# Optimization experiments

Measured on AMD Instinct MI355X. Metric: run time of the kernel, lower is better.

## Reference

```python
import jax, jax.numpy as jnp
import numpy as np

EMBED_DIM = 1024
NUM_HEADS = 16
HEAD_DIM = EMBED_DIM // NUM_HEADS
LN_EPS = 1e-5


def setup_inputs() -> dict:
    key = jax.random.key(0)
    ks = jax.random.split(key, 6)
    b, s, d = 2, 2048, EMBED_DIM
    scale = 1.0 / np.sqrt(d)
    x = jax.random.normal(ks[0], (b, s, d), dtype=jnp.float32)
    w_qkv = jax.random.normal(ks[1], (d, 3 * d), dtype=jnp.float32) * scale
    b_qkv = jax.random.normal(ks[2], (3 * d,), dtype=jnp.float32) * 0.02
    w_out = jax.random.normal(ks[3], (d, d), dtype=jnp.float32) * scale
    b_out = jax.random.normal(ks[4], (d,), dtype=jnp.float32) * 0.02
    gamma = jnp.ones((d,), dtype=jnp.float32)
    ln_beta = jnp.zeros((d,), dtype=jnp.float32)
    beta = jax.random.normal(ks[5], (), dtype=jnp.float32) * 0.1
    return {"x": x, "w_qkv": w_qkv, "b_qkv": b_qkv, "w_out": w_out,
            "b_out": b_out, "gamma": gamma, "ln_beta": ln_beta, "beta": beta}


def _layernorm(x, gamma, ln_beta):
    mu = jnp.mean(x, axis=-1, keepdims=True)
    var = jnp.mean(jnp.square(x - mu), axis=-1, keepdims=True)
    return (x - mu) * jax.lax.rsqrt(var + LN_EPS) * gamma + ln_beta


def reference(x, w_qkv, b_qkv, w_out, b_out, gamma, ln_beta, beta):
    b, s, d = x.shape
    h, hd = NUM_HEADS, HEAD_DIM
    residual = x
    xn = _layernorm(x, gamma, ln_beta)
    qkv = xn @ w_qkv + b_qkv                       # [b, s, 3d]
    qkv = qkv.reshape(b, s, 3, h, hd)
    q = jnp.transpose(qkv[:, :, 0], (0, 2, 1, 3))  # [b, h, s, hd]
    k = jnp.transpose(qkv[:, :, 1], (0, 2, 1, 3))
    v = jnp.transpose(qkv[:, :, 2], (0, 2, 1, 3))
    attn = jnp.einsum('bhqd,bhkd->bhqk', q, k) / np.sqrt(hd)
    idx = jnp.arange(s)
    dist = jnp.abs(idx[None, :] - idx[:, None]).astype(attn.dtype)  # [s, s]
    attn = attn + beta * jnp.log1p(dist)[None, None, :, :]
    probs = jax.nn.softmax(attn, axis=-1)
    ctx = jnp.einsum('bhqk,bhkd->bhqd', probs, v)  # [b, h, s, hd]
    ctx = jnp.transpose(ctx, (0, 2, 1, 3)).reshape(b, s, d)
    return residual + ctx @ w_out + b_out
```

## Files before the change

kernel.cpp:

```cpp
#include <hip/hip_runtime.h>

#define SEQ 2048
#define DIM 1024
#define NHEAD 16
#define HDIM 64
#define NTOK 4096
#define N3D 3072

typedef __attribute__((ext_vector_type(8))) short bf16x8;
typedef __attribute__((ext_vector_type(4))) float floatx4;
typedef __attribute__((ext_vector_type(4))) unsigned short ushortx4;

__device__ __forceinline__ unsigned short f2bf(float f) {
    unsigned int u = __builtin_bit_cast(unsigned int, f);
    u += 0x7FFFu + ((u >> 16) & 1u);
    return (unsigned short)(u >> 16);
}

__device__ __forceinline__ void async_copy16(const void* g, const void* l) {
    __builtin_amdgcn_global_load_lds(
        (const __attribute__((address_space(1))) unsigned int*)(unsigned long long)g,
        (__attribute__((address_space(3))) unsigned int*)(unsigned int)(unsigned long long)l,
        16, 0, 0);
}

#define MFMA_BF16(a, b, c) __builtin_amdgcn_mfma_f32_16x16x32_bf16((a), (b), (c), 0, 0, 0)

__global__ __launch_bounds__(256)
void prep_kernel(const float* __restrict__ w_qkv, unsigned short* __restrict__ wqkvT,
                 const float* __restrict__ w_out, unsigned short* __restrict__ woutT,
                 const float* __restrict__ x, const float* __restrict__ gamma,
                 const float* __restrict__ lnb, unsigned short* __restrict__ xn,
                 const float* __restrict__ betap, float* __restrict__ logt_g) {
    const int bid = blockIdx.x;
    const int tid = threadIdx.x;
    if (bid >= 8192) {
        const float betaV = betap[0];
        const float L2E = 1.44269504f;
        int i = (bid - 8192) * 256 + tid;
        logt_g[i] = betaV * log1pf((float)i) * L2E - 20.0f;
        logt_g[i + 1024] = betaV * log1pf((float)(i + 1024)) * L2E - 20.0f;
        return;
    }
    if (bid < 4096) {
        __shared__ float tile[32][33];
        const float* src; unsigned short* dst; int cols, bx, by;
        if (bid < 3072) { src = w_qkv; dst = wqkvT; cols = N3D; bx = bid % 96; by = bid / 96; }
        else { int t = bid - 3072; src = w_out; dst = woutT; cols = DIM; bx = t & 31; by = t >> 5; }
        const int c0 = bx * 32, r0 = by * 32;
        const int tx = tid & 31, ty = tid >> 5;
        for (int i = 0; i < 4; ++i) {
            int r = ty + i * 8;
            tile[r][tx] = src[(size_t)(r0 + r) * cols + c0 + tx];
        }
        __syncthreads();
        for (int i = 0; i < 4; ++i) {
            int rr = ty + i * 8;
            dst[(size_t)(c0 + rr) * DIM + r0 + tx] = f2bf(tile[tx][rr]);
        }
    } else {
        const int row = bid - 4096;
        const float* xr = x + (size_t)row * DIM;
        float4 v = ((const float4*)xr)[tid];
        float s = v.x + v.y + v.z + v.w;
        float s2 = v.x * v.x + v.y * v.y + v.z * v.z + v.w * v.w;
        for (int off = 1; off < 64; off <<= 1) {
            s += __shfl_xor(s, off, 64);
            s2 += __shfl_xor(s2, off, 64);
        }
        __shared__ float red[8];
        const int wave = tid >> 6, lane = tid & 63;
        if (lane == 0) { red[wave] = s; red[4 + wave] = s2; }
        __syncthreads();
        s = red[0] + red[1] + red[2] + red[3];
        s2 = red[4] + red[5] + red[6] + red[7];
        const float mu = s * (1.0f / DIM);
        const float var = s2 * (1.0f / DIM) - mu * mu;
        const float rstd = rsqrtf(var + 1e-5f);
        float4 g = ((const float4*)gamma)[tid];
        float4 bb = ((const float4*)lnb)[tid];
        unsigned short* o = xn + (size_t)row * DIM + tid * 4;
        o[0] = f2bf((v.x - mu) * rstd * g.x + bb.x);
        o[1] = f2bf((v.y - mu) * rstd * g.y + bb.y);
        o[2] = f2bf((v.z - mu) * rstd * g.z + bb.z);
        o[3] = f2bf((v.w - mu) * rstd * g.w + bb.w);
    }
}

__global__ __launch_bounds__(256)
void qkv_gemm(const unsigned short* __restrict__ A, const unsigned short* __restrict__ Bt,
              const float* __restrict__ bias, unsigned short* __restrict__ qo,
              unsigned short* __restrict__ ko, unsigned short* __restrict__ vTo) {
    __shared__ unsigned short Asm[2][128 * 64];
    __shared__ unsigned short Bsm[2][192 * 64];
    const int tid = threadIdx.x;
    const int wave = tid >> 6, lane = tid & 63;
    const int quad = lane >> 4, r16 = lane & 15;
    const int flat = blockIdx.x;
    const int xcd = flat & 7, c = flat >> 3;
    const int mt = (xcd >> 1) * 8 + (c >> 3);
    const int nt = (xcd & 1) * 8 + (c & 7);
    const int m0 = mt * 128, n0 = nt * 192;
    const int wm = (wave & 1) * 64, wn = (wave >> 1) * 96;
    floatx4 acc[4][6] = {};
    for (int p = 0; p < 4; ++p) {
        int s = tid + p * 256;
        async_copy16(A + (size_t)(m0 + (s >> 3)) * DIM + ((s & 7) << 3), &Asm[0][s * 8]);
    }
    for (int p = 0; p < 6; ++p) {
        int s = tid + p * 256;
        async_copy16(Bt + (size_t)(n0 + (s >> 3)) * DIM + ((s & 7) << 3), &Bsm[0][s * 8]);
    }
    __syncthreads();
    for (int it = 0; it < 16; ++it) {
        const int cur = it & 1;
        if (it + 1 < 16) {
            const int k1 = (it + 1) * 64;
            for (int p = 0; p < 4; ++p) {
                int s = tid + p * 256;
                async_copy16(A + (size_t)(m0 + (s >> 3)) * DIM + k1 + ((s & 7) << 3),
                             &Asm[cur ^ 1][s * 8]);
            }
            for (int p = 0; p < 6; ++p) {
                int s = tid + p * 256;
                async_copy16(Bt + (size_t)(n0 + (s >> 3)) * DIM + k1 + ((s & 7) << 3),
                             &Bsm[cur ^ 1][s * 8]);
            }
        }
        for (int h = 0; h < 2; ++h) {
            bf16x8 af[4], bfr[6];
            for (int i = 0; i < 4; ++i)
                af[i] = *(const bf16x8*)(&Asm[cur][(wm + i * 16 + r16) * 64 + h * 32 + quad * 8]);
            for (int j = 0; j < 6; ++j)
                bfr[j] = *(const bf16x8*)(&Bsm[cur][(wn + j * 16 + r16) * 64 + h * 32 + quad * 8]);
            for (int i = 0; i < 4; ++i)
                for (int j = 0; j < 6; ++j)
                    acc[i][j] = MFMA_BF16(af[i], bfr[j], acc[i][j]);
        }
        __syncthreads();
    }
    for (int j = 0; j < 6; ++j) {
        int n = n0 + wn + j * 16 + r16;
        float bn = bias[n];
        int part = n >> 10, nn = n & 1023;
        int head = nn >> 6, hdi = nn & 63;
        for (int i = 0; i < 4; ++i) {
            int mbase = m0 + wm + i * 16 + quad * 4;
            int bIdx = mbase >> 11, sIdx = mbase & 2047;
            if (part == 2) {
                ushortx4 pack;
                for (int e = 0; e < 4; ++e) pack[e] = f2bf(acc[i][j][e] + bn);
                *(ushortx4*)(vTo + ((size_t)(bIdx * NHEAD + head) * HDIM + hdi) * SEQ + sIdx) = pack;
            } else {
                unsigned short* dst = (part == 0) ? qo : ko;
                for (int e = 0; e < 4; ++e)
                    dst[((size_t)(bIdx * NHEAD + head) * SEQ + sIdx + e) * HDIM + hdi] =
                        f2bf(acc[i][j][e] + bn);
            }
        }
    }
}

__global__ __launch_bounds__(512)
void attn_kernel(const unsigned short* __restrict__ qg, const unsigned short* __restrict__ kg,
                 const unsigned short* __restrict__ vTg, const float* __restrict__ logt,
                 unsigned short* __restrict__ ctx) {
    __shared__ unsigned short QP[128][72];
    __shared__ unsigned short Kd[2][64 * 64];
    __shared__ unsigned short Vd[2][64 * 64];

    const int tid = threadIdx.x;
    const int wave = tid >> 6, lane = tid & 63;
    const int quad = lane >> 4, r16 = lane & 15;
    const int flat = blockIdx.y * 16 + blockIdx.x;
    const int swz = (flat & 7) * 64 + (flat >> 3);
    const int bh = swz >> 4, qt = swz & 15;
    const int qBase = qt * 128;
    const float L2E = 1.44269504f;
    const float c1 = 0.125f * L2E;

    const unsigned short* qptr = qg + ((size_t)bh * SEQ + qBase) * HDIM;
    for (int s = tid; s < 1024; s += 512) {
        int r = s >> 3, c8 = (s & 7) << 3;
        *(bf16x8*)(&QP[r][c8]) = *(const bf16x8*)(qptr + r * HDIM + c8);
    }

    const int sr = tid >> 3;
    const int scg = (tid & 7) ^ (sr & 7);
    const unsigned short* kbh = kg + (size_t)bh * SEQ * HDIM;
    const unsigned short* vbh = vTg + (size_t)bh * HDIM * SEQ;
    async_copy16(kbh + (size_t)sr * HDIM + scg * 8, &Kd[0][tid * 8]);
    async_copy16(vbh + (size_t)sr * SEQ + scg * 8, &Vd[0][tid * 8]);
    __syncthreads();

    bf16x8 qf0 = *(const bf16x8*)(&QP[wave * 16 + r16][quad * 8]);
    bf16x8 qf1 = *(const bf16x8*)(&QP[wave * 16 + r16][32 + quad * 8]);

    const bf16x8 onesv = {0x3F80, 0x3F80, 0x3F80, 0x3F80, 0x3F80, 0x3F80, 0x3F80, 0x3F80};

    floatx4 o[5] = {};
    const int qWaveBase = qBase + wave * 16;
    const int qrT = qWaveBase + r16;

    for (int kt0 = 0; kt0 < SEQ; kt0 += 64) {
        const int buf = (kt0 >> 6) & 1;
        if (kt0 + 64 < SEQ) {
            async_copy16(kbh + (size_t)(kt0 + 64 + sr) * HDIM + scg * 8, &Kd[buf ^ 1][tid * 8]);
            async_copy16(vbh + (size_t)sr * SEQ + kt0 + 64 + scg * 8, &Vd[buf ^ 1][tid * 8]);
        }

        floatx4 sc[4];
        __builtin_amdgcn_s_setprio(1);
        for (int ct = 0; ct < 4; ++ct) {
            int rK = ct * 16 + r16;
            const unsigned short* kb = &Kd[buf][rK * 64];
            bf16x8 kf0 = *(const bf16x8*)(kb + ((quad ^ (rK & 7)) << 3));
            bf16x8 kf1 = *(const bf16x8*)(kb + (((quad ^ 4) ^ (rK & 7)) << 3));
            floatx4 z = {0.f, 0.f, 0.f, 0.f};
            z = MFMA_BF16(kf0, qf0, z);
            z = MFMA_BF16(kf1, qf1, z);
            sc[ct] = z;
        }
        __builtin_amdgcn_s_setprio(0);
        for (int ct = 0; ct < 4; ++ct) {
            const int keyTile = kt0 + ct * 16;
            const int kbase = keyTile + quad * 4;
            if (qWaveBase >= keyTile + 16) {
                const float* lp = &logt[qrT - kbase - 3];
                for (int i = 0; i < 4; ++i)
                    sc[ct][i] = __builtin_amdgcn_exp2f(sc[ct][i] * c1 + lp[3 - i]);
            } else if (keyTile >= qWaveBase + 16) {
                const float* lp = &logt[kbase - qrT];
                for (int i = 0; i < 4; ++i)
                    sc[ct][i] = __builtin_amdgcn_exp2f(sc[ct][i] * c1 + lp[i]);
            } else {
                for (int i = 0; i < 4; ++i) {
                    int dist = qrT - (kbase + i);
                    dist = dist < 0 ? -dist : dist;
                    sc[ct][i] = __builtin_amdgcn_exp2f(sc[ct][i] * c1 + logt[dist]);
                }
            }
        }
        {
            unsigned short* prow = &QP[wave * 16 + r16][0];
            for (int ct = 0; ct < 4; ++ct) {
                unsigned int lo, hi;
                asm("v_cvt_pk_bf16_f32 %0, %1, %2" : "=v"(lo) : "v"(sc[ct][0]), "v"(sc[ct][1]));
                asm("v_cvt_pk_bf16_f32 %0, %1, %2" : "=v"(hi) : "v"(sc[ct][2]), "v"(sc[ct][3]));
                uint2 pk; pk.x = lo; pk.y = hi;
                *(uint2*)(prow + ct * 16 + quad * 4) = pk;
            }
        }
        bf16x8 pf0 = *(const bf16x8*)(&QP[wave * 16 + r16][quad * 8]);
        bf16x8 pf1 = *(const bf16x8*)(&QP[wave * 16 + r16][32 + quad * 8]);
        __builtin_amdgcn_s_setprio(1);
        for (int nt = 0; nt < 4; ++nt) {
            int rV = nt * 16 + r16;
            const unsigned short* vb = &Vd[buf][rV * 64];
            bf16x8 vf0 = *(const bf16x8*)(vb + ((quad ^ (rV & 7)) << 3));
            bf16x8 vf1 = *(const bf16x8*)(vb + (((quad ^ 4) ^ (rV & 7)) << 3));
            o[nt] = MFMA_BF16(pf0, vf0, o[nt]);
            o[nt] = MFMA_BF16(pf1, vf1, o[nt]);
        }
        o[4] = MFMA_BF16(pf0, onesv, o[4]);
        o[4] = MFMA_BF16(pf1, onesv, o[4]);
        __builtin_amdgcn_s_setprio(0);

        __syncthreads();
    }

    const int b_ = bh >> 4, h_ = bh & 15;
    for (int i = 0; i < 4; ++i) {
        float inv = 1.0f / o[4][i];
        int qi = qBase + wave * 16 + quad * 4 + i;
        for (int nt = 0; nt < 4; ++nt) {
            int d = nt * 16 + r16;
            ctx[((size_t)(b_ * SEQ + qi)) * DIM + h_ * HDIM + d] = f2bf(o[nt][i] * inv);
        }
    }
}

__global__ __launch_bounds__(256)
void out_gemm(const unsigned short* __restrict__ A, const unsigned short* __restrict__ Bt,
              const float* __restrict__ bias, const float* __restrict__ resid,
              float* __restrict__ out) {
    __shared__ unsigned short Asm[2][128 * 64];
    __shared__ unsigned short Bsm[2][64 * 64];
    const int tid = threadIdx.x;
    const int wave = tid >> 6, lane = tid & 63;
    const int quad = lane >> 4, r16 = lane & 15;
    const int flat = blockIdx.y * 16 + blockIdx.x;
    const int swz = (flat & 7) * 64 + (flat >> 3);
    const int m0 = (swz >> 4) * 128, n0 = (swz & 15) * 64;
    const int wm = (wave & 1) * 64, wn = (wave >> 1) * 32;
    floatx4 acc[4][2] = {};
    for (int p = 0; p < 4; ++p) {
        int s = tid + p * 256;
        async_copy16(A + (size_t)(m0 + (s >> 3)) * DIM + ((s & 7) << 3), &Asm[0][s * 8]);
    }
    for (int p = 0; p < 2; ++p) {
        int s = tid + p * 256;
        async_copy16(Bt + (size_t)(n0 + (s >> 3)) * DIM + ((s & 7) << 3), &Bsm[0][s * 8]);
    }
    __syncthreads();
    for (int it = 0; it < 16; ++it) {
        const int cur = it & 1;
        if (it + 1 < 16) {
            const int k1 = (it + 1) * 64;
            for (int p = 0; p < 4; ++p) {
                int s = tid + p * 256;
                async_copy16(A + (size_t)(m0 + (s >> 3)) * DIM + k1 + ((s & 7) << 3),
                             &Asm[cur ^ 1][s * 8]);
            }
            for (int p = 0; p < 2; ++p) {
                int s = tid + p * 256;
                async_copy16(Bt + (size_t)(n0 + (s >> 3)) * DIM + k1 + ((s & 7) << 3),
                             &Bsm[cur ^ 1][s * 8]);
            }
        }
        for (int h = 0; h < 2; ++h) {
            bf16x8 af[4], bfr[2];
            for (int i = 0; i < 4; ++i)
                af[i] = *(const bf16x8*)(&Asm[cur][(wm + i * 16 + r16) * 64 + h * 32 + quad * 8]);
            for (int j = 0; j < 2; ++j)
                bfr[j] = *(const bf16x8*)(&Bsm[cur][(wn + j * 16 + r16) * 64 + h * 32 + quad * 8]);
            for (int i = 0; i < 4; ++i)
                for (int j = 0; j < 2; ++j)
                    acc[i][j] = MFMA_BF16(af[i], bfr[j], acc[i][j]);
        }
        __syncthreads();
    }
    for (int i = 0; i < 4; ++i)
        for (int j = 0; j < 2; ++j)
            for (int e = 0; e < 4; ++e) {
                int m = m0 + wm + i * 16 + quad * 4 + e;
                int n = n0 + wn + j * 16 + r16;
                out[(size_t)m * DIM + n] = acc[i][j][e] + bias[n] + resid[(size_t)m * DIM + n];
            }
}

extern "C" void kernel_launch(void* const* d_in, const int* in_sizes, int n_in,
                              void* d_out, int out_size, void* d_ws, size_t ws_size,
                              hipStream_t stream) {
    const float* x     = (const float*)d_in[0];
    const float* w_qkv = (const float*)d_in[1];
    const float* b_qkv = (const float*)d_in[2];
    const float* w_out = (const float*)d_in[3];
    const float* b_out = (const float*)d_in[4];
    const float* gamma = (const float*)d_in[5];
    const float* ln_b  = (const float*)d_in[6];
    const float* beta  = (const float*)d_in[7];
    float* out = (float*)d_out;

    char* ws = (char*)d_ws;
    const size_t MB = 1u << 20;
    unsigned short* xn    = (unsigned short*)(ws);
    unsigned short* wqkvT = (unsigned short*)(ws + 8 * MB);
    unsigned short* woutT = (unsigned short*)(ws + 14 * MB);
    unsigned short* qb    = (unsigned short*)(ws + 16 * MB);
    unsigned short* kb    = (unsigned short*)(ws + 24 * MB);
    unsigned short* vTb   = (unsigned short*)(ws + 32 * MB);
    float* logt_g         = (float*)(ws + 40 * MB);
    unsigned short* ctx   = xn;

    prep_kernel<<<8196, 256, 0, stream>>>(w_qkv, wqkvT, w_out, woutT, x, gamma, ln_b, xn,
                                          beta, logt_g);
    qkv_gemm<<<512, 256, 0, stream>>>(xn, wqkvT, b_qkv, qb, kb, vTb);
    attn_kernel<<<dim3(SEQ / 128, 32), 512, 0, stream>>>(qb, kb, vTb, logt_g, ctx);
    out_gemm<<<dim3(16, 32), 256, 0, stream>>>(ctx, woutT, b_out, x, out);
}
```

Before: 219.0 us.

## Shrink attention blocks to 64 query rows and swizzle the P scratch buffer

After: 224.0 us. +2.3%, slower.

```diff
diff --git a/kernel.cpp b/kernel.cpp
--- a/kernel.cpp
+++ b/kernel.cpp
@@ -161,52 +161,56 @@
     }
 }
 
-__global__ __launch_bounds__(512)
+__global__ __launch_bounds__(256)
 void attn_kernel(const unsigned short* __restrict__ qg, const unsigned short* __restrict__ kg,
                  const unsigned short* __restrict__ vTg, const float* __restrict__ logt,
                  unsigned short* __restrict__ ctx) {
-    __shared__ unsigned short QP[128][72];
+    __shared__ unsigned short QP[64][64];
     __shared__ unsigned short Kd[2][64 * 64];
     __shared__ unsigned short Vd[2][64 * 64];
 
     const int tid = threadIdx.x;
     const int wave = tid >> 6, lane = tid & 63;
     const int quad = lane >> 4, r16 = lane & 15;
-    const int flat = blockIdx.y * 16 + blockIdx.x;
-    const int swz = (flat & 7) * 64 + (flat >> 3);
-    const int bh = swz >> 4, qt = swz & 15;
-    const int qBase = qt * 128;
+    const int flat = blockIdx.x;
+    const int swz = (flat & 7) * 128 + (flat >> 3);
+    const int bh = swz >> 5, qt = swz & 31;
+    const int qBase = qt * 64;
     const float L2E = 1.44269504f;
     const float c1 = 0.125f * L2E;
 
     const unsigned short* qptr = qg + ((size_t)bh * SEQ + qBase) * HDIM;
-    for (int s = tid; s < 1024; s += 512) {
-        int r = s >> 3, c8 = (s & 7) << 3;
-        *(bf16x8*)(&QP[r][c8]) = *(const bf16x8*)(qptr + r * HDIM + c8);
-    }
-
-    const int sr = tid >> 3;
-    const int scg = (tid & 7) ^ (sr & 7);
+    const int qrow = wave * 16 + r16;
+    bf16x8 qf0 = *(const bf16x8*)(qptr + qrow * HDIM + quad * 8);
+    bf16x8 qf1 = *(const bf16x8*)(qptr + qrow * HDIM + 32 + quad * 8);
+
     const unsigned short* kbh = kg + (size_t)bh * SEQ * HDIM;
     const unsigned short* vbh = vTg + (size_t)bh * HDIM * SEQ;
-    async_copy16(kbh + (size_t)sr * HDIM + scg * 8, &Kd[0][tid * 8]);
-    async_copy16(vbh + (size_t)sr * SEQ + scg * 8, &Vd[0][tid * 8]);
+    for (int p = 0; p < 2; ++p) {
+        int s = tid + p * 256;
+        int sr = s >> 3, scg = (s & 7) ^ (sr & 7);
+        async_copy16(kbh + (size_t)sr * HDIM + scg * 8, &Kd[0][s * 8]);
+        async_copy16(vbh + (size_t)sr * SEQ + scg * 8, &Vd[0][s * 8]);
+    }
     __syncthreads();
-
-    bf16x8 qf0 = *(const bf16x8*)(&QP[wave * 16 + r16][quad * 8]);
-    bf16x8 qf1 = *(const bf16x8*)(&QP[wave * 16 + r16][32 + quad * 8]);
 
     const bf16x8 onesv = {0x3F80, 0x3F80, 0x3F80, 0x3F80, 0x3F80, 0x3F80, 0x3F80, 0x3F80};
 
     floatx4 o[5] = {};
     const int qWaveBase = qBase + wave * 16;
     const int qrT = qWaveBase + r16;
+    const int rx = r16 & 7;
+    unsigned short* prow = &QP[wave * 16 + r16][0];
 
     for (int kt0 = 0; kt0 < SEQ; kt0 += 64) {
         const int buf = (kt0 >> 6) & 1;
         if (kt0 + 64 < SEQ) {
-            async_copy16(kbh + (size_t)(kt0 + 64 + sr) * HDIM + scg * 8, &Kd[buf ^ 1][tid * 8]);
-            async_copy16(vbh + (size_t)sr * SEQ + kt0 + 64 + scg * 8, &Vd[buf ^ 1][tid * 8]);
+            for (int p = 0; p < 2; ++p) {
+                int s = tid + p * 256;
+                int sr = s >> 3, scg = (s & 7) ^ (sr & 7);
+                async_copy16(kbh + (size_t)(kt0 + 64 + sr) * HDIM + scg * 8, &Kd[buf ^ 1][s * 8]);
+                async_copy16(vbh + (size_t)sr * SEQ + kt0 + 64 + scg * 8, &Vd[buf ^ 1][s * 8]);
+            }
         }
 
         floatx4 sc[4];
@@ -241,18 +245,16 @@
                 }
             }
         }
-        {
-            unsigned short* prow = &QP[wave * 16 + r16][0];
-            for (int ct = 0; ct < 4; ++ct) {
-                unsigned int lo, hi;
-                asm("v_cvt_pk_bf16_f32 %0, %1, %2" : "=v"(lo) : "v"(sc[ct][0]), "v"(sc[ct][1]));
-                asm("v_cvt_pk_bf16_f32 %0, %1, %2" : "=v"(hi) : "v"(sc[ct][2]), "v"(sc[ct][3]));
-                uint2 pk; pk.x = lo; pk.y = hi;
-                *(uint2*)(prow + ct * 16 + quad * 4) = pk;
-            }
-        }
-        bf16x8 pf0 = *(const bf16x8*)(&QP[wave * 16 + r16][quad * 8]);
-        bf16x8 pf1 = *(const bf16x8*)(&QP[wave * 16 + r16][32 + quad * 8]);
+        for (int ct = 0; ct < 4; ++ct) {
+            unsigned int lo, hi;
+            asm("v_cvt_pk_bf16_f32 %0, %1, %2" : "=v"(lo) : "v"(sc[ct][0]), "v"(sc[ct][1]));
+            asm("v_cvt_pk_bf16_f32 %0, %1, %2" : "=v"(hi) : "v"(sc[ct][2]), "v"(sc[ct][3]));
+            uint2 pk; pk.x = lo; pk.y = hi;
+            int slot = (2 * ct + (quad >> 1)) ^ rx;
+            *(uint2*)((char*)prow + slot * 16 + (quad & 1) * 8) = pk;
+        }
+        bf16x8 pf0 = *(const bf16x8*)((const char*)prow + ((quad ^ rx) * 16));
+        bf16x8 pf1 = *(const bf16x8*)((const char*)prow + (((4 + quad) ^ rx) * 16));
         __builtin_amdgcn_s_setprio(1);
         for (int nt = 0; nt < 4; ++nt) {
             int rV = nt * 16 + r16;
@@ -366,6 +368,6 @@
     prep_kernel<<<8196, 256, 0, stream>>>(w_qkv, wqkvT, w_out, woutT, x, gamma, ln_b, xn,
                                           beta, logt_g);
     qkv_gemm<<<512, 256, 0, stream>>>(xn, wqkvT, b_qkv, qb, kb, vTb);
-    attn_kernel<<<dim3(SEQ / 128, 32), 512, 0, stream>>>(qb, kb, vTb, logt_g, ctx);
+    attn_kernel<<<1024, 256, 0, stream>>>(qb, kb, vTb, logt_g, ctx);
     out_gemm<<<dim3(16, 32), 256, 0, stream>>>(ctx, woutT, b_out, x, out);
 }
```
